# Kernel tuning notes

Hardware: AMD Instinct MI355X
Metric: run time of the kernel (lower is better)

## Reference

```python
import jax, jax.numpy as jnp
import numpy as np


def setup_inputs() -> dict:
    key = jax.random.key(0)
    k1, k2, k3 = jax.random.split(key, 3)
    B, M, N, D = 8, 12, 32, 256
    C = N * N          # Conv2d channel dim == N*N (see permute/view in source)
    R = 2              # reduction
    x = jax.random.normal(k1, (B, M, N, D), dtype=jnp.float32)
    W1 = jax.random.normal(k2, (C // R, C), dtype=jnp.float32) * 0.02  # Conv2d(C, C//R, 1, bias=False)
    W2 = jax.random.normal(k3, (C, C // R), dtype=jnp.float32) * 0.02  # Conv2d(C//R, C, 1, bias=False)
    return {"x": x, "W1": W1, "W2": W2}


def _mycorr(x):
    # Pearson correlation across feature dim D -> [B, M, N, N] adjacency
    xm = x - x.mean(axis=-1, keepdims=True)
    cov = jnp.einsum('bmnd,bmkd->bmnk', xm, xm)
    diag = jnp.diagonal(cov, axis1=-2, axis2=-1)                 # [B, M, N]
    norm = jnp.sqrt(jnp.clip(diag, 1e-12))
    return cov / (norm[..., :, None] * norm[..., None, :])


def reference(x, W1, W2):
    B, M, N, D = x.shape
    adj = _mycorr(x)

    # Fused pairwise-combo + mean over concat dim (2D):
    #   cat([Wh_i, pos_ij * Wh_j], -1).mean(-1) = (sum_d Wh_i + sum_d pos_ij*Wh_j) / (2D)
    # pos_ij[d] = 1 where Wh_i[d] == Wh_j[d] else 2   (source's where(diff==0, 1, 2))
    Wi = x[:, :, :, None, :]          # [B, M, N, 1, D]
    Wj = x[:, :, None, :, :]          # [B, M, 1, N, D]
    pos = jnp.where(Wi == Wj, jnp.float32(1.0), jnp.float32(2.0))
    e0 = (x.sum(-1)[:, :, :, None] + (pos * Wj).sum(-1)) / (2.0 * D)  # [B, M, N, N]

    # squeeze-excite style 1x1-conv MLP over the N*N channel dim
    ef = e0.reshape(B, M, N * N).transpose(0, 2, 1)                   # [B, C=N*N, M]
    h = jax.nn.relu(jnp.einsum('oc,bcm->bom', W1, ef))                # [B, C//R, M]
    e2 = jnp.einsum('co,bom->bcm', W2, h)                             # [B, C, M]
    e = jax.nn.sigmoid(e2.transpose(0, 2, 1).reshape(B, M, N, N))

    att = jnp.where(adj > 0, e, jnp.float32(-1e12))
    att = jax.nn.softmax(att, axis=-1)
    return jnp.einsum('bmnk,bmkd->bmnd', att, x)
```

## Files before the change

### kernel.cpp

```cpp
#include <hip/hip_runtime.h>


#define NGRP 12

__device__ unsigned int g_bar0[NGRP * 32];
__device__ unsigned int g_bar1[NGRP * 32];
__device__ unsigned int g_done[NGRP * 32];

__device__ __forceinline__ float dot4(float4 a, float4 b) {
    return a.x*b.x + a.y*b.y + a.z*b.z + a.w*b.w;
}
__device__ __forceinline__ void fma4(float4& acc, float s, float4 v) {
    acc.x += s*v.x; acc.y += s*v.y; acc.z += s*v.z; acc.w += s*v.w;
}

__device__ __forceinline__ void st_agent(float* p, float v) {
    __hip_atomic_store(p, v, __ATOMIC_RELAXED, __HIP_MEMORY_SCOPE_AGENT);
}
__device__ __forceinline__ float ld_agent(const float* p) {
    return __hip_atomic_load(p, __ATOMIC_RELAXED, __HIP_MEMORY_SCOPE_AGENT);
}
__device__ __forceinline__ unsigned long long ld_agent64(const unsigned long long* p) {
    return __hip_atomic_load(p, __ATOMIC_RELAXED, __HIP_MEMORY_SCOPE_AGENT);
}

__device__ __forceinline__ void bar_arrive(unsigned int* ctr) {
    __syncthreads();
    if (threadIdx.x == 0)
        __hip_atomic_fetch_add(ctr, 1u, __ATOMIC_RELAXED, __HIP_MEMORY_SCOPE_AGENT);
}
__device__ __forceinline__ void bar_wait(unsigned int* ctr) {
    if (threadIdx.x == 0) {
        while (__hip_atomic_load(ctr, __ATOMIC_RELAXED, __HIP_MEMORY_SCOPE_AGENT) < 16u)
            __builtin_amdgcn_s_sleep(2);
    }
    __syncthreads();
}

__global__ __launch_bounds__(512) void fused(
        const float* __restrict__ x, const float* __restrict__ W1,
        const float* __restrict__ W2, float* __restrict__ out,
        float* __restrict__ W1A, float* __restrict__ Ssum,
        float* __restrict__ Et)
{
    __shared__ float4 xs4[32][65];
    __shared__ float  w[16][1024];
    __shared__ float  hl[8][512];
    __shared__ float  att[32][36];
    __shared__ float  S_l8[8][32];
    __shared__ float  S_loc[32];
    const int t = threadIdx.x;
    const int bid = blockIdx.x;
    const int g = bid >> 4;
    const int gi = g * 32;
    const int bm = bid >> 1, hh = bid & 1;
    const float4* x4 = (const float4*)x;

    #pragma unroll
    for (int i = 0; i < 4; ++i) {
        int idx = t + 512*i;
        xs4[idx >> 6][idx & 63] = x4[bm*2048 + idx];
    }
    __syncthreads();
    {
        int r = t >> 4, dq = t & 15;
        float s = 0.f;
        #pragma unroll
        for (int j = 0; j < 4; ++j) {
            float4 v = xs4[r][dq + 16*j];
            s += v.x + v.y + v.z + v.w;
        }
        s += __shfl_xor(s, 1, 16);
        s += __shfl_xor(s, 2, 16);
        s += __shfl_xor(s, 4, 16);
        s += __shfl_xor(s, 8, 16);
        if (dq == 0) S_loc[r] = s;
    }
    __syncthreads();
    if (hh == 0 && t < 32) st_agent(&Ssum[bm*32 + t], S_loc[t]);
    {
        const int oT = bid & 15;
        #pragma unroll
        for (int rnd = 0; rnd < 2; ++rnd) {
            const float4* W14 = (const float4*)(W1 + (oT*32 + rnd*16)*1024);
            float4* w4 = (float4*)&w[0][0];
            #pragma unroll
            for (int i = 0; i < 8; ++i) w4[t + 512*i] = W14[t + 512*i];
            __syncthreads();
            const int ol = t >> 5, n = t & 31;
            const float* row = &w[ol][0];
            float T1 = 0.f, T2 = 0.f;
            #pragma unroll
            for (int k = 0; k < 32; ++k) T1 += row[n*32 + ((k + n) & 31)];
            #pragma unroll
            for (int m = 0; m < 32; ++m) T2 += row[m*32 + n];
            float diag = row[n*33];
            st_agent(&W1A[(oT*32 + rnd*16 + ol)*32 + n],
                     (T1 + 2.f*T2 - diag) * (1.f/512.f));
            __syncthreads();
        }
    }
    bar_arrive(&g_bar0[gi]);

    const int ga = t >> 4, gb = t & 15;
    float g00=0.f, g01=0.f, g10=0.f, g11=0.f;
    float sa0=0.f, sa1=0.f, sb0=0.f, sb1=0.f;
    if (t < 256) {
        #pragma unroll 8
        for (int q = 0; q < 64; ++q) {
            float4 a0 = xs4[ga][q],    a1 = xs4[ga+16][q];
            float4 b0 = xs4[gb][q],    b1 = xs4[gb+16][q];
            g00 += dot4(a0,b0); g01 += dot4(a0,b1);
            g10 += dot4(a1,b0); g11 += dot4(a1,b1);
        }
        sa0 = S_loc[ga]    * (1.f/256.f);
        sa1 = S_loc[ga+16] * (1.f/256.f);
        sb0 = S_loc[gb];
        sb1 = S_loc[gb+16];
    }
    bar_wait(&g_bar0[gi]);

    {
        if (t < 256) ((float*)S_l8)[t] = ld_agent(&Ssum[g*256 + t]);
        __syncthreads();
        {
            const unsigned long long* wrow =
                (const unsigned long long*)(W1A + t*32);
            float wv[32];
            #pragma unroll
            for (int i = 0; i < 16; ++i) {
                unsigned long long v = ld_agent64(wrow + i);
                wv[2*i]   = __uint_as_float((unsigned)(v & 0xffffffffu));
                wv[2*i+1] = __uint_as_float((unsigned)(v >> 32));
            }
            #pragma unroll
            for (int bl = 0; bl < 8; ++bl) {
                const float* sb = &S_l8[bl][0];
                float a = 0.f;
                #pragma unroll
                for (int n = 0; n < 32; ++n) a += wv[n] * sb[n];
                hl[bl][t] = fmaxf(a, 0.f);
            }
        }
        __syncthreads();
        const int cQ = bid & 15;
        const int olane = t & 31, cgp = t >> 5;
        const int c0 = cQ*64 + cgp;
        const float4* w4a = (const float4*)(W2 + (c0     )*512);
        const float4* w4b = (const float4*)(W2 + (c0 + 16)*512);
        const float4* w4c = (const float4*)(W2 + (c0 + 32)*512);
        const float4* w4d = (const float4*)(W2 + (c0 + 48)*512);
        float accA[8] = {0.f,0.f,0.f,0.f,0.f,0.f,0.f,0.f};
        float accB[8] = {0.f,0.f,0.f,0.f,0.f,0.f,0.f,0.f};
        float accC[8] = {0.f,0.f,0.f,0.f,0.f,0.f,0.f,0.f};
        float accD[8] = {0.f,0.f,0.f,0.f,0.f,0.f,0.f,0.f};
        #pragma unroll
        for (int oo = 0; oo < 4; ++oo) {
            float4 hv[8];
            #pragma unroll
            for (int bl = 0; bl < 8; ++bl)
                hv[bl] = *((const float4*)&hl[bl][(oo*32 + olane)*4]);
            float4 wa = w4a[oo*32 + olane];
            float4 wb = w4b[oo*32 + olane];
            float4 wc = w4c[oo*32 + olane];
            float4 wd = w4d[oo*32 + olane];
            #pragma unroll
            for (int bl = 0; bl < 8; ++bl) {
                accA[bl] += dot4(wa, hv[bl]);
                accB[bl] += dot4(wb, hv[bl]);
                accC[bl] += dot4(wc, hv[bl]);
                accD[bl] += dot4(wd, hv[bl]);
            }
        }
        #pragma unroll
        for (int bl = 0; bl < 8; ++bl) {
            float a = accA[bl], b = accB[bl], c = accC[bl], d = accD[bl];
            #pragma unroll
            for (int m = 1; m < 32; m <<= 1) {
                a += __shfl_xor(a, m, 32);
                b += __shfl_xor(b, m, 32);
                c += __shfl_xor(c, m, 32);
                d += __shfl_xor(d, m, 32);
            }
            accA[bl]=a; accB[bl]=b; accC[bl]=c; accD[bl]=d;
        }
        if (olane == 0) {
            #pragma unroll
            for (int bl = 0; bl < 8; ++bl) {
                int row = (g*8 + bl)*1024;
                st_agent(&Et[row + c0],      1.f/(1.f + __expf(-accA[bl])));
                st_agent(&Et[row + c0 + 16], 1.f/(1.f + __expf(-accB[bl])));
                st_agent(&Et[row + c0 + 32], 1.f/(1.f + __expf(-accC[bl])));
                st_agent(&Et[row + c0 + 48], 1.f/(1.f + __expf(-accD[bl])));
            }
        }
    }
    bar_arrive(&g_bar1[gi]);
    bar_wait(&g_bar1[gi]);

    if (t < 256) {
        const float* Eb = Et + bm*1024;
        float e00 = ld_agent(&Eb[ga*32 + gb]);
        float e01 = ld_agent(&Eb[ga*32 + gb+16]);
        float e10 = ld_agent(&Eb[(ga+16)*32 + gb]);
        float e11 = ld_agent(&Eb[(ga+16)*32 + gb+16]);
        att[ga][gb]       = (g00 - sa0*sb0) > 0.f ? e00 : -1e12f;
        att[ga][gb+16]    = (g01 - sa0*sb1) > 0.f ? e01 : -1e12f;
        att[ga+16][gb]    = (g10 - sa1*sb0) > 0.f ? e10 : -1e12f;
        att[ga+16][gb+16] = (g11 - sa1*sb1) > 0.f ? e11 : -1e12f;
    }
    __syncthreads();
    {
        int r = t >> 4, q = t & 15;
        float2 lg = *((const float2*)&att[r][q*2]);
        float m = fmaxf(lg.x, lg.y);
        m = fmaxf(m, __shfl_xor(m,1,16));
        m = fmaxf(m, __shfl_xor(m,2,16));
        m = fmaxf(m, __shfl_xor(m,4,16));
        m = fmaxf(m, __shfl_xor(m,8,16));
        float2 p;
        p.x = __expf(lg.x-m); p.y = __expf(lg.y-m);
        float s = p.x + p.y;
        s += __shfl_xor(s,1,16);
        s += __shfl_xor(s,2,16);
        s += __shfl_xor(s,4,16);
        s += __shfl_xor(s,8,16);
        float inv = 1.f/s;
        p.x*=inv; p.y*=inv;
        *((float2*)&att[r][q*2]) = p;
    }
    __syncthreads();
    {
        int txl = t & 31, wy = t >> 5;
        int r0 = wy*2;
        float4 acc0={0,0,0,0}, acc1={0,0,0,0};
        #pragma unroll
        for (int kq = 0; kq < 8; ++kq) {
            float4 xa = xs4[kq*4+0][hh*32 + txl];
            float4 xb = xs4[kq*4+1][hh*32 + txl];
            float4 xc = xs4[kq*4+2][hh*32 + txl];
            float4 xd = xs4[kq*4+3][hh*32 + txl];
            float4 w0 = *((const float4*)&att[r0+0][kq*4]);
            float4 w1 = *((const float4*)&att[r0+1][kq*4]);
            fma4(acc0,w0.x,xa); fma4(acc0,w0.y,xb); fma4(acc0,w0.z,xc); fma4(acc0,w0.w,xd);
            fma4(acc1,w1.x,xa); fma4(acc1,w1.y,xb); fma4(acc1,w1.z,xc); fma4(acc1,w1.w,xd);
        }
        float4* out4 = (float4*)out;
        int base = bm*2048 + hh*32 + txl;
        out4[base + (r0+0)*64] = acc0;
        out4[base + (r0+1)*64] = acc1;
    }

    if (t == 0) {
        unsigned int old = __hip_atomic_fetch_add(&g_done[gi], 1u,
                              __ATOMIC_RELAXED, __HIP_MEMORY_SCOPE_AGENT);
        if (old == 15u) {
            __hip_atomic_store(&g_bar0[gi], 0u, __ATOMIC_RELAXED, __HIP_MEMORY_SCOPE_AGENT);
            __hip_atomic_store(&g_bar1[gi], 0u, __ATOMIC_RELAXED, __HIP_MEMORY_SCOPE_AGENT);
            __hip_atomic_store(&g_done[gi], 0u, __ATOMIC_RELAXED, __HIP_MEMORY_SCOPE_AGENT);
        }
    }
}

extern "C" void kernel_launch(void* const* d_in, const int* in_sizes, int n_in,
                              void* d_out, int out_size, void* d_ws, size_t ws_size,
                              hipStream_t stream) {
    const float* x  = (const float*)d_in[0];
    const float* W1 = (const float*)d_in[1];
    const float* W2 = (const float*)d_in[2];
    float* out = (float*)d_out;
    float* ws  = (float*)d_ws;

    float* W1A  = ws;
    float* Ssum = ws + 16384;
    float* Et   = ws + 19456;

    fused<<<192, 512, 0, stream>>>(x, W1, W2, out, W1A, Ssum, Et);
}
```

Measured before the change: 88.43 us.

## Split x tile across block pair and exchange partial Gram and row sums

Each of the two blocks sharing a (b,m) slice now loads only its half of the feature dimension into shared memory, halving x traffic per block and the LDS footprint. The Gram matrix and the row sums are computed on the half, written to global workspace, and combined with the partner block's partials after the existing grid barrier. This removes duplicate work and loads in exchange for extra global stores and loads of partial results.

Result: faster. 86.01 us (-2.7%).

```diff
diff --git a/kernel.cpp b/kernel.cpp
--- a/kernel.cpp
+++ b/kernel.cpp
@@ -40,10 +40,10 @@
 __global__ __launch_bounds__(512) void fused(
         const float* __restrict__ x, const float* __restrict__ W1,
         const float* __restrict__ W2, float* __restrict__ out,
-        float* __restrict__ W1A, float* __restrict__ Ssum,
-        float* __restrict__ Et)
+        float* __restrict__ W1A, float* __restrict__ SsumH,
+        float* __restrict__ Et, float* __restrict__ pg)
 {
-    __shared__ float4 xs4[32][65];
+    __shared__ float4 xs4[32][33];
     __shared__ float  w[16][1024];
     __shared__ float  hl[8][512];
     __shared__ float  att[32][36];
@@ -54,19 +54,21 @@
     const int g = bid >> 4;
     const int gi = g * 32;
     const int bm = bid >> 1, hh = bid & 1;
+    const int lbl = (bid & 15) >> 1;
     const float4* x4 = (const float4*)x;
 
     #pragma unroll
-    for (int i = 0; i < 4; ++i) {
+    for (int i = 0; i < 2; ++i) {
         int idx = t + 512*i;
-        xs4[idx >> 6][idx & 63] = x4[bm*2048 + idx];
+        int row = idx >> 5, c4 = idx & 31;
+        xs4[row][c4] = x4[bm*2048 + row*64 + hh*32 + c4];
     }
     __syncthreads();
     {
         int r = t >> 4, dq = t & 15;
         float s = 0.f;
         #pragma unroll
-        for (int j = 0; j < 4; ++j) {
+        for (int j = 0; j < 2; ++j) {
             float4 v = xs4[r][dq + 16*j];
             s += v.x + v.y + v.z + v.w;
         }
@@ -77,7 +79,7 @@
         if (dq == 0) S_loc[r] = s;
     }
     __syncthreads();
-    if (hh == 0 && t < 32) st_agent(&Ssum[bm*32 + t], S_loc[t]);
+    if (t < 32) st_agent(&SsumH[hh*3072 + bm*32 + t], S_loc[t]);
     {
         const int oT = bid & 15;
         #pragma unroll
@@ -104,24 +106,28 @@
 
     const int ga = t >> 4, gb = t & 15;
     float g00=0.f, g01=0.f, g10=0.f, g11=0.f;
-    float sa0=0.f, sa1=0.f, sb0=0.f, sb1=0.f;
     if (t < 256) {
         #pragma unroll 8
-        for (int q = 0; q < 64; ++q) {
+        for (int q = 0; q < 32; ++q) {
             float4 a0 = xs4[ga][q],    a1 = xs4[ga+16][q];
             float4 b0 = xs4[gb][q],    b1 = xs4[gb+16][q];
             g00 += dot4(a0,b0); g01 += dot4(a0,b1);
             g10 += dot4(a1,b0); g11 += dot4(a1,b1);
         }
-        sa0 = S_loc[ga]    * (1.f/256.f);
-        sa1 = S_loc[ga+16] * (1.f/256.f);
-        sb0 = S_loc[gb];
-        sb1 = S_loc[gb+16];
+        float* pgb = pg + bid*1024;
+        st_agent(&pgb[ga*32 + gb],          g00);
+        st_agent(&pgb[ga*32 + gb+16],       g01);
+        st_agent(&pgb[(ga+16)*32 + gb],     g10);
+        st_agent(&pgb[(ga+16)*32 + gb+16],  g11);
     }
     bar_wait(&g_bar0[gi]);
 
     {
-        if (t < 256) ((float*)S_l8)[t] = ld_agent(&Ssum[g*256 + t]);
+        if (t < 256) {
+            int bl = t >> 5, rr = t & 31;
+            int o = (g*8 + bl)*32 + rr;
+            S_l8[bl][rr] = ld_agent(&SsumH[o]) + ld_agent(&SsumH[3072 + o]);
+        }
         __syncthreads();
         {
             const unsigned long long* wrow =
@@ -199,6 +205,14 @@
     bar_wait(&g_bar1[gi]);
 
     if (t < 256) {
+        const float* pgs = pg + (bid ^ 1)*1024;
+        g00 += ld_agent(&pgs[ga*32 + gb]);
+        g01 += ld_agent(&pgs[ga*32 + gb+16]);
+        g10 += ld_agent(&pgs[(ga+16)*32 + gb]);
+        g11 += ld_agent(&pgs[(ga+16)*32 + gb+16]);
+        float sa0 = S_l8[lbl][ga]    * (1.f/256.f);
+        float sa1 = S_l8[lbl][ga+16] * (1.f/256.f);
+        float sb0 = S_l8[lbl][gb], sb1 = S_l8[lbl][gb+16];
         const float* Eb = Et + bm*1024;
         float e00 = ld_agent(&Eb[ga*32 + gb]);
         float e01 = ld_agent(&Eb[ga*32 + gb+16]);
@@ -236,10 +250,10 @@
         float4 acc0={0,0,0,0}, acc1={0,0,0,0};
         #pragma unroll
         for (int kq = 0; kq < 8; ++kq) {
-            float4 xa = xs4[kq*4+0][hh*32 + txl];
-            float4 xb = xs4[kq*4+1][hh*32 + txl];
-            float4 xc = xs4[kq*4+2][hh*32 + txl];
-            float4 xd = xs4[kq*4+3][hh*32 + txl];
+            float4 xa = xs4[kq*4+0][txl];
+            float4 xb = xs4[kq*4+1][txl];
+            float4 xc = xs4[kq*4+2][txl];
+            float4 xd = xs4[kq*4+3][txl];
             float4 w0 = *((const float4*)&att[r0+0][kq*4]);
             float4 w1 = *((const float4*)&att[r0+1][kq*4]);
             fma4(acc0,w0.x,xa); fma4(acc0,w0.y,xb); fma4(acc0,w0.z,xc); fma4(acc0,w0.w,xd);
@@ -271,9 +285,10 @@
     float* out = (float*)d_out;
     float* ws  = (float*)d_ws;
 
-    float* W1A  = ws;
-    float* Ssum = ws + 16384;
-    float* Et   = ws + 19456;
-
-    fused<<<192, 512, 0, stream>>>(x, W1, W2, out, W1A, Ssum, Et);
-}
+    float* W1A   = ws;
+    float* SsumH = ws + 16384;
+    float* Et    = ws + 22528;
+    float* pg    = ws + 120832;
+
+    fused<<<192, 512, 0, stream>>>(x, W1, W2, out, W1A, SsumH, Et, pg);
+}
```
